# Performance work log

Measured on AMD Instinct MI355X. Metric: run time of the kernel, lower is better.

## Reference

```python
import jax, jax.numpy as jnp
import numpy as np

N = 33554432  # number of flattened prediction/target points (~128 MB fp32 each)


def setup_inputs() -> dict:
    key = jax.random.key(0)
    k1, k2 = jax.random.split(key)
    predicted = jax.random.uniform(k1, (N,), dtype=jnp.float32)
    target = jax.random.uniform(k2, (N,), dtype=jnp.float32)
    weights = jnp.array([1.0, 2.0, 4.0, 8.0, 16.0], dtype=jnp.float32)
    edge = jnp.array([0.0, 0.1, 0.25, 0.5, 0.75, 1.0], dtype=jnp.float32)
    return {"predicted": predicted, "target": target, "weights": weights, "edge": edge}


def reference(predicted, target, weights, edge):
    # Original loops over bins: elements with edge[i] < t <= edge[i+1] get weight[i];
    # elements outside (edge[0], edge[-1]] are DROPPED (weight 0).
    nbins = weights.shape[0]
    # digitize(..., right=True): returns i s.t. edge[i-1] < t <= edge[i]; shift to bin index
    bin_idx = jnp.digitize(target, edge, right=True) - 1  # [N] int
    valid = (bin_idx >= 0) & (bin_idx < nbins)
    w = jnp.where(valid, weights[jnp.clip(bin_idx, 0, nbins - 1)], 0.0)
    loss = jnp.sum(w * (predicted - target) ** 2) / jnp.sum(weights)
    return loss
```

## Files before the change

### kernel.cpp

```cpp
#include <hip/hip_runtime.h>


__device__ __forceinline__ float wmse_elem(float p, float t,
                                           float e0, float e1, float e2,
                                           float e3, float e4, float e5,
                                           float w0, float w1, float w2,
                                           float w3, float w4) {
    float w = 0.0f;
    w = (t > e0 && t <= e1) ? w0 : w;
    w = (t > e1 && t <= e2) ? w1 : w;
    w = (t > e2 && t <= e3) ? w2 : w;
    w = (t > e3 && t <= e4) ? w3 : w;
    w = (t > e4 && t <= e5) ? w4 : w;
    float d = p - t;
    return w * d * d;
}

#define WMSE4(p, t) (                                                          \
    wmse_elem((p).x, (t).x, e0, e1, e2, e3, e4, e5, w0, w1, w2, w3, w4) +      \
    wmse_elem((p).y, (t).y, e0, e1, e2, e3, e4, e5, w0, w1, w2, w3, w4) +      \
    wmse_elem((p).z, (t).z, e0, e1, e2, e3, e4, e5, w0, w1, w2, w3, w4) +      \
    wmse_elem((p).w, (t).w, e0, e1, e2, e3, e4, e5, w0, w1, w2, w3, w4))

#define PER_BLOCK_F4 2048LL

__global__ __launch_bounds__(256) void WeightedMSELoss_60335700574782_kernel(
    const float* __restrict__ pred, const float* __restrict__ targ,
    const float* __restrict__ edge, const float* __restrict__ weights,
    float* __restrict__ partial) {
    const float e0 = edge[0], e1 = edge[1], e2 = edge[2];
    const float e3 = edge[3], e4 = edge[4], e5 = edge[5];
    const float w0 = weights[0], w1 = weights[1], w2 = weights[2];
    const float w3 = weights[3], w4 = weights[4];

    const float4* __restrict__ p4 = (const float4*)pred;
    const float4* __restrict__ t4 = (const float4*)targ;
    const long long base = (long long)blockIdx.x * PER_BLOCK_F4 + threadIdx.x;

    float4 pa = p4[base + 0 * 256];
    float4 ta = t4[base + 0 * 256];
    float4 pb = p4[base + 1 * 256];
    float4 tb = t4[base + 1 * 256];
    float4 pc = p4[base + 2 * 256];
    float4 tc = t4[base + 2 * 256];
    float4 pd = p4[base + 3 * 256];
    float4 td = t4[base + 3 * 256];
    float4 pe = p4[base + 4 * 256];
    float4 te = t4[base + 4 * 256];
    float4 pf = p4[base + 5 * 256];
    float4 tf = t4[base + 5 * 256];
    float4 pg = p4[base + 6 * 256];
    float4 tg = t4[base + 6 * 256];
    float4 ph = p4[base + 7 * 256];
    float4 th = t4[base + 7 * 256];

    float acc0 = WMSE4(pa, ta) + WMSE4(pe, te);
    float acc1 = WMSE4(pb, tb) + WMSE4(pf, tf);
    float acc2 = WMSE4(pc, tc) + WMSE4(pg, tg);
    float acc3 = WMSE4(pd, td) + WMSE4(ph, th);
    float acc = (acc0 + acc1) + (acc2 + acc3);

    #pragma unroll
    for (int off = 32; off > 0; off >>= 1)
        acc += __shfl_down(acc, off, 64);

    __shared__ float smem[4];
    const int lane = threadIdx.x & 63;
    const int wid = threadIdx.x >> 6;
    if (lane == 0) smem[wid] = acc;
    __syncthreads();
    if (threadIdx.x == 0)
        partial[blockIdx.x] = smem[0] + smem[1] + smem[2] + smem[3];
}

__global__ __launch_bounds__(256) void wmse_finish_kernel(
    const float* __restrict__ partial, int nparts,
    const float* __restrict__ pred, const float* __restrict__ targ,
    const float* __restrict__ edge, const float* __restrict__ weights,
    float* __restrict__ out, long long tail_start, long long n) {
    const float e0 = edge[0], e1 = edge[1], e2 = edge[2];
    const float e3 = edge[3], e4 = edge[4], e5 = edge[5];
    const float w0 = weights[0], w1 = weights[1], w2 = weights[2];
    const float w3 = weights[3], w4 = weights[4];
    const float inv_wsum = 1.0f / (w0 + w1 + w2 + w3 + w4);

    float acc = 0.0f;
    for (int i = threadIdx.x; i < nparts; i += blockDim.x)
        acc += partial[i];

    for (long long j = tail_start + threadIdx.x; j < n; j += blockDim.x)
        acc += wmse_elem(pred[j], targ[j], e0, e1, e2, e3, e4, e5, w0, w1, w2, w3, w4);

    #pragma unroll
    for (int off = 32; off > 0; off >>= 1)
        acc += __shfl_down(acc, off, 64);

    __shared__ float smem[4];
    const int lane = threadIdx.x & 63;
    const int wid = threadIdx.x >> 6;
    if (lane == 0) smem[wid] = acc;
    __syncthreads();
    if (threadIdx.x == 0)
        out[0] = (smem[0] + smem[1] + smem[2] + smem[3]) * inv_wsum;
}

extern "C" void kernel_launch(void* const* d_in, const int* in_sizes, int n_in,
                              void* d_out, int out_size, void* d_ws, size_t ws_size,
                              hipStream_t stream) {
    const float* pred    = (const float*)d_in[0];
    const float* targ    = (const float*)d_in[1];
    const float* weights = (const float*)d_in[2];
    const float* edge    = (const float*)d_in[3];
    float* out = (float*)d_out;
    float* partial = (float*)d_ws;
    const long long n = (long long)in_sizes[0];
    const long long n4 = n >> 2;

    const int grid = (int)(n4 / PER_BLOCK_F4);
    const long long tail_start = (long long)grid * PER_BLOCK_F4 * 4;

    if (grid > 0) {
        WeightedMSELoss_60335700574782_kernel<<<grid, 256, 0, stream>>>(
            pred, targ, edge, weights, partial);
    }
    wmse_finish_kernel<<<1, 256, 0, stream>>>(
        partial, grid, pred, targ, edge, weights, out, tail_start, n);
}
```

Baseline: 284.0 us.

## Issue loads via inline asm with staged vmcnt waits and halve per-thread work

Replaces compiler-generated loads with hand-written global_load_dwordx4 inline assembly, issued in interleaved pred/target order, then waits on vmcnt in stages so computation on the first chunk can overlap the remaining loads. Per-thread work drops from 8 to 4 float4 pairs, doubling the grid and the number of partial sums the finish kernel must reduce. Less data is in flight per thread, which may or may not be offset by higher occupancy. The inline asm skips compiler-inserted waits, so correctness depends on the manual vmcnt counts being right.

```diff
diff --git a/kernel.cpp b/kernel.cpp
--- a/kernel.cpp
+++ b/kernel.cpp
@@ -1,5 +1,12 @@
 #include <hip/hip_runtime.h>
+#include <stdint.h>
 
+
+typedef float f32x4 __attribute__((ext_vector_type(4)));
+
+#define BLOCK 256
+#define F4PT 4
+#define F4PB (BLOCK * F4PT)
 
 __device__ __forceinline__ float wmse_elem(float p, float t,
                                            float e0, float e1, float e2,
@@ -16,13 +23,11 @@
     return w * d * d;
 }
 
-#define WMSE4(p, t) (                                                          \
-    wmse_elem((p).x, (t).x, e0, e1, e2, e3, e4, e5, w0, w1, w2, w3, w4) +      \
-    wmse_elem((p).y, (t).y, e0, e1, e2, e3, e4, e5, w0, w1, w2, w3, w4) +      \
-    wmse_elem((p).z, (t).z, e0, e1, e2, e3, e4, e5, w0, w1, w2, w3, w4) +      \
-    wmse_elem((p).w, (t).w, e0, e1, e2, e3, e4, e5, w0, w1, w2, w3, w4))
-
-#define PER_BLOCK_F4 2048LL
+#define WMSE4V(p, t) (                                                         \
+    wmse_elem((p)[0], (t)[0], e0, e1, e2, e3, e4, e5, w0, w1, w2, w3, w4) +    \
+    wmse_elem((p)[1], (t)[1], e0, e1, e2, e3, e4, e5, w0, w1, w2, w3, w4) +    \
+    wmse_elem((p)[2], (t)[2], e0, e1, e2, e3, e4, e5, w0, w1, w2, w3, w4) +    \
+    wmse_elem((p)[3], (t)[3], e0, e1, e2, e3, e4, e5, w0, w1, w2, w3, w4))
 
 __global__ __launch_bounds__(256) void WeightedMSELoss_60335700574782_kernel(
     const float* __restrict__ pred, const float* __restrict__ targ,
@@ -33,31 +38,42 @@
     const float w0 = weights[0], w1 = weights[1], w2 = weights[2];
     const float w3 = weights[3], w4 = weights[4];
 
-    const float4* __restrict__ p4 = (const float4*)pred;
-    const float4* __restrict__ t4 = (const float4*)targ;
-    const long long base = (long long)blockIdx.x * PER_BLOCK_F4 + threadIdx.x;
+    const f32x4* __restrict__ p4 = (const f32x4*)pred;
+    const f32x4* __restrict__ t4 = (const f32x4*)targ;
+    const long long base = (long long)blockIdx.x * F4PB + threadIdx.x;
 
-    float4 pa = p4[base + 0 * 256];
-    float4 ta = t4[base + 0 * 256];
-    float4 pb = p4[base + 1 * 256];
-    float4 tb = t4[base + 1 * 256];
-    float4 pc = p4[base + 2 * 256];
-    float4 tc = t4[base + 2 * 256];
-    float4 pd = p4[base + 3 * 256];
-    float4 td = t4[base + 3 * 256];
-    float4 pe = p4[base + 4 * 256];
-    float4 te = t4[base + 4 * 256];
-    float4 pf = p4[base + 5 * 256];
-    float4 tf = t4[base + 5 * 256];
-    float4 pg = p4[base + 6 * 256];
-    float4 tg = t4[base + 6 * 256];
-    float4 ph = p4[base + 7 * 256];
-    float4 th = t4[base + 7 * 256];
+    const f32x4* pa = p4 + base;
+    const f32x4* ta = t4 + base;
 
-    float acc0 = WMSE4(pa, ta) + WMSE4(pe, te);
-    float acc1 = WMSE4(pb, tb) + WMSE4(pf, tf);
-    float acc2 = WMSE4(pc, tc) + WMSE4(pg, tg);
-    float acc3 = WMSE4(pd, td) + WMSE4(ph, th);
+    f32x4 P0, P1, P2, P3, T0, T1, T2, T3;
+    asm volatile(
+        "global_load_dwordx4 %0, %8, off\n\t"
+        "global_load_dwordx4 %4, %12, off\n\t"
+        "global_load_dwordx4 %1, %9, off\n\t"
+        "global_load_dwordx4 %5, %13, off\n\t"
+        "global_load_dwordx4 %2, %10, off\n\t"
+        "global_load_dwordx4 %6, %14, off\n\t"
+        "global_load_dwordx4 %3, %11, off\n\t"
+        "global_load_dwordx4 %7, %15, off"
+        : "=&v"(P0), "=&v"(P1), "=&v"(P2), "=&v"(P3),
+          "=&v"(T0), "=&v"(T1), "=&v"(T2), "=&v"(T3)
+        : "v"(pa), "v"(pa + 256), "v"(pa + 512), "v"(pa + 768),
+          "v"(ta), "v"(ta + 256), "v"(ta + 512), "v"(ta + 768));
+
+    float acc0, acc1, acc2, acc3;
+    asm volatile("s_waitcnt vmcnt(6)" ::: "memory");
+    __builtin_amdgcn_sched_barrier(0);
+    acc0 = WMSE4V(P0, T0);
+    asm volatile("s_waitcnt vmcnt(4)" ::: "memory");
+    __builtin_amdgcn_sched_barrier(0);
+    acc1 = WMSE4V(P1, T1);
+    asm volatile("s_waitcnt vmcnt(2)" ::: "memory");
+    __builtin_amdgcn_sched_barrier(0);
+    acc2 = WMSE4V(P2, T2);
+    asm volatile("s_waitcnt vmcnt(0)" ::: "memory");
+    __builtin_amdgcn_sched_barrier(0);
+    acc3 = WMSE4V(P3, T3);
+
     float acc = (acc0 + acc1) + (acc2 + acc3);
 
     #pragma unroll
@@ -116,13 +132,13 @@
     const long long n = (long long)in_sizes[0];
     const long long n4 = n >> 2;
 
-    const int grid = (int)(n4 / PER_BLOCK_F4);
-    const long long tail_start = (long long)grid * PER_BLOCK_F4 * 4;
+    const int grid = (int)(n4 / F4PB);
+    const long long tail_start = (long long)grid * F4PB * 4;
 
     if (grid > 0) {
-        WeightedMSELoss_60335700574782_kernel<<<grid, 256, 0, stream>>>(
+        WeightedMSELoss_60335700574782_kernel<<<grid, BLOCK, 0, stream>>>(
             pred, targ, edge, weights, partial);
     }
-    wmse_finish_kernel<<<1, 256, 0, stream>>>(
+    wmse_finish_kernel<<<1, BLOCK, 0, stream>>>(
         partial, grid, pred, targ, edge, weights, out, tail_start, n);
 }
```

Result: no change. 285.2 us (+0.4%).
